# Kernel tuning notes

Hardware: AMD Instinct MI355X
Metric: run time of the kernel (lower is better)

## Reference

```python
import jax, jax.numpy as jnp
import numpy as np

N = 50000
E = 400000
D = 128   # embed_dim == per-head out_channels
H = 2     # graph_heads
NEG_SLOPE = 0.2


def setup_inputs() -> dict:
    key = jax.random.key(0)
    ks = jax.random.split(key, 10)
    s = 1.0 / np.sqrt(D)
    x = jax.random.normal(ks[0], (N, D), dtype=jnp.float32)
    edge_index = jax.random.randint(ks[1], (2, E), 0, N, dtype=jnp.int64)
    # GATv2Conv params: lin_l (source), lin_r (target), attention vector, conv bias
    Wl = jax.random.uniform(ks[2], (H * D, D), jnp.float32, -s, s)
    bl = jax.random.uniform(ks[3], (H * D,), jnp.float32, -s, s)
    Wr = jax.random.uniform(ks[4], (H * D, D), jnp.float32, -s, s)
    br = jax.random.uniform(ks[5], (H * D,), jnp.float32, -s, s)
    att = jax.random.uniform(ks[6], (H, D), jnp.float32, -s, s)
    bias_conv = jnp.zeros((H * D,), jnp.float32)
    # trailing Linear(H*D -> D)
    so = 1.0 / np.sqrt(H * D)
    Wo = jax.random.uniform(ks[7], (D, H * D), jnp.float32, -so, so)
    bo = jax.random.uniform(ks[8], (D,), jnp.float32, -so, so)
    return {"x": x, "edge_index": edge_index, "Wl": Wl, "bl": bl, "Wr": Wr,
            "br": br, "att": att, "bias_conv": bias_conv, "Wo": Wo, "bo": bo}


def reference(x, edge_index, Wl, bl, Wr, br, att, bias_conv, Wo, bo):
    n = x.shape[0]
    # GATv2Conv default add_self_loops=True
    loops = jnp.arange(n, dtype=edge_index.dtype)
    src = jnp.concatenate([edge_index[0], loops])  # x_j (source / message)
    dst = jnp.concatenate([edge_index[1], loops])  # x_i (target / aggregation)

    xl = (x @ Wl.T + bl).reshape(n, H, D)  # source projection
    xr = (x @ Wr.T + br).reshape(n, H, D)  # target projection

    e = xl[src] + xr[dst]                               # [E+N, H, D]
    score = jnp.einsum('ehd,hd->eh', jax.nn.leaky_relu(e, NEG_SLOPE), att)

    # segment softmax over destination neighborhoods
    m = jax.ops.segment_max(score, dst, num_segments=n)  # [N, H]
    a = jnp.exp(score - m[dst])
    denom = jax.ops.segment_sum(a, dst, num_segments=n)
    alpha = a / (denom[dst] + 1e-16)                     # [E+N, H]

    out = jax.ops.segment_sum(xl[src] * alpha[..., None], dst, num_segments=n)
    out = out.reshape(n, H * D) + bias_conv              # concat heads + conv bias
    return out @ Wo.T + bo                               # [N, D]
```

## Files before the change

kernel.cpp:

```cpp
#include <hip/hip_runtime.h>
#include <math.h>

#define DIMV 128
#define HDV  256
#define NEGS 0.2f
#define CAPV 64

typedef __attribute__((ext_vector_type(8))) short short8;
typedef __attribute__((ext_vector_type(8))) unsigned short ushort8v;
typedef __attribute__((ext_vector_type(4))) float f32x4;

__device__ __forceinline__ int edge_at(const int* p, int is64, long long idx) {
    return is64 ? p[2 * idx] : p[(size_t)idx];
}

__device__ __forceinline__ unsigned short f2bf(float f) {
    union { float f; unsigned u; } v; v.f = f;
    unsigned r = (v.u + 0x7FFF + ((v.u >> 16) & 1)) >> 16;
    return (unsigned short)r;
}
__device__ __forceinline__ float bf2f(unsigned short b) {
    union { unsigned u; float f; } v; v.u = ((unsigned)b) << 16;
    return v.f;
}

__global__ __launch_bounds__(256) void build_kernel(
    const int* __restrict__ eidx, int E, int nn,
    int* __restrict__ deg, int* __restrict__ elist)
{
    const int idx = blockIdx.x * 256 + threadIdx.x;
    const int Et = E + nn;
    if (idx >= Et) return;
    const int is64 = ((eidx[1] | eidx[3] | eidx[5] | eidx[7]) == 0) ? 1 : 0;
    int s, d;
    if (idx < E) {
        s = edge_at(eidx, is64, idx);
        d = edge_at(eidx, is64, (long long)E + idx);
    } else {
        s = idx - E; d = s;
    }
    int pos = atomicAdd(deg + d, 1);
    if (pos < CAPV) elist[(size_t)d * CAPV + pos] = s;
}

__global__ __launch_bounds__(256) void prep_kernel(
    const float* __restrict__ Wl, const float* __restrict__ Wr,
    const float* __restrict__ Wo,
    unsigned short* __restrict__ WB, unsigned short* __restrict__ WoB)
{
    const int b = blockIdx.x, t = threadIdx.x;
    if (b < 128) {
        int tid = b * 256 + t;
        int f = tid * 2;
        int e    = f & 7;
        int rowc = (f >> 3) & 127;
        int lg   = (f >> 10) & 3;
        int kk   = (f >> 12) & 3;
        int mh   = f >> 14;
        int mat = mh >> 1, half = mh & 1;
        const float* W = mat ? Wr : Wl;
        float2 v = *(const float2*)(W + (size_t)(half * 128 + rowc) * DIMV + kk * 32 + lg * 8 + e);
        ushort2 o; o.x = f2bf(v.x); o.y = f2bf(v.y);
        *(ushort2*)(WB + f) = o;
    } else {
        int tid = (b - 128) * 256 + t;
        int f = tid * 2;
        int e    = f & 7;
        int rowc = (f >> 3) & 127;
        int lg   = (f >> 10) & 3;
        int kk   = f >> 12;
        float2 v = *(const float2*)(Wo + (size_t)rowc * HDV + kk * 32 + lg * 8 + e);
        ushort2 o; o.x = f2bf(v.x); o.y = f2bf(v.y);
        *(ushort2*)(WoB + f) = o;
    }
}

__global__ __launch_bounds__(512) void proj_mfma_kernel(
    const float* __restrict__ x,
    const unsigned short* __restrict__ WB,
    const float* __restrict__ bl, const float* __restrict__ br,
    unsigned short* __restrict__ xl, unsigned short* __restrict__ xr, int nn)
{
    __shared__ unsigned short xs[64 * 128];
    const int t = threadIdx.x;
    const int m0b = blockIdx.x * 64;
    char* xsb = (char*)xs;

    for (int i = t; i < 64 * 32; i += 512) {
        int rr = i >> 5, q = i & 31;
        float4 v = make_float4(0.f, 0.f, 0.f, 0.f);
        if (m0b + rr < nn) v = ((const float4*)(x + (size_t)(m0b + rr) * DIMV))[q];
        ushort4 bv; bv.x = f2bf(v.x); bv.y = f2bf(v.y); bv.z = f2bf(v.z); bv.w = f2bf(v.w);
        *(ushort4*)(xsb + (((rr * 256) + q * 8) ^ ((rr & 7) << 4))) = bv;
    }
    __syncthreads();

    const int lane = t & 63, w8 = t >> 6;
    const int w = w8 & 3, half = w8 >> 2;
    const int lm = lane & 15, lg = lane >> 4;
    f32x4 acc0[8], acc1[8];
#pragma unroll
    for (int nt = 0; nt < 8; ++nt) {
        acc0[nt] = (f32x4){0.f, 0.f, 0.f, 0.f};
        acc1[nt] = (f32x4){0.f, 0.f, 0.f, 0.f};
    }

    const int arow = w * 16 + lm;
    const int aswz = (arow & 7) << 4;
#pragma unroll
    for (int kk = 0; kk < 4; ++kk) {
        const int koff = kk * 64 + lg * 16;
        short8 afrag = *(const short8*)(xsb + ((arow * 256 + koff) ^ aswz));
        const unsigned short* wb0 = WB + (size_t)(((half * 4 + kk) * 4 + lg) * 128) * 8;
        const unsigned short* wb1 = WB + (size_t)((((2 + half) * 4 + kk) * 4 + lg) * 128) * 8;
#pragma unroll
        for (int nt = 0; nt < 8; ++nt) {
            const int brow = nt * 16 + lm;
            short8 b0 = *(const short8*)(wb0 + brow * 8);
            acc0[nt] = __builtin_amdgcn_mfma_f32_16x16x32_bf16(afrag, b0, acc0[nt], 0, 0, 0);
            short8 b1 = *(const short8*)(wb1 + brow * 8);
            acc1[nt] = __builtin_amdgcn_mfma_f32_16x16x32_bf16(afrag, b1, acc1[nt], 0, 0, 0);
        }
    }

    const int colbase = half * 128;
#pragma unroll
    for (int nt = 0; nt < 8; ++nt) {
        const int c = colbase + nt * 16 + lm;
        const float bv0 = bl[c], bv1 = br[c];
#pragma unroll
        for (int rg = 0; rg < 4; ++rg) {
            const int node = m0b + w * 16 + lg * 4 + rg;
            if (node < nn) {
                xl[(size_t)node * HDV + c] = f2bf(acc0[nt][rg] + bv0);
                xr[(size_t)node * HDV + c] = f2bf(acc1[nt][rg] + bv1);
            }
        }
    }
}

__global__ __launch_bounds__(256) void fused_kernel(
    const unsigned short* __restrict__ xl, const unsigned short* __restrict__ xr,
    const float* __restrict__ att,
    const int* __restrict__ deg, const int* __restrict__ elist,
    const float* __restrict__ bias_conv,
    unsigned short* __restrict__ aggb, int nn)
{
    const int t = threadIdx.x, lane = t & 63, wid = t >> 6;
    const int h = lane & 31, par = lane >> 5;
    const int n0 = blockIdx.x * 16;
    float att8[8], bc8[8];
#pragma unroll
    for (int k = 0; k < 8; ++k) {
        att8[k] = att[h * 8 + k];
        bc8[k]  = bias_conv[h * 8 + k];
    }

    for (int j = 0; j < 4; ++j) {
        const int n = n0 + wid * 4 + j;
        int dg = 0;
        const int* __restrict__ row = elist;
        float xr8[8];
#pragma unroll
        for (int k = 0; k < 8; ++k) xr8[k] = 0.f;
        if (n < nn) {
            dg = min(deg[n], CAPV);
            row = elist + (size_t)n * CAPV;
            ushort8v v = *(const ushort8v*)(xr + (size_t)n * HDV + h * 8);
#pragma unroll
            for (int k = 0; k < 8; ++k) xr8[k] = bf2f(v[k]);
        }
        const int myidx = row[lane];
        const int np = (dg + 1) >> 1, np1 = np - 1, dgm1 = dg - 1;
        float m0 = -1e30f, den = 0.f;
        float a8[8];
#pragma unroll
        for (int k = 0; k < 8; ++k) a8[k] = 0.f;

        if (np > 0) {
            int i0 = __shfl(myidx, min(par, dgm1), 64);
            int i1 = __shfl(myidx, min(2 * min(1, np1) + par, dgm1), 64);
            int i2 = __shfl(myidx, min(2 * min(2, np1) + par, dgm1), 64);
            int i3 = __shfl(myidx, min(2 * min(3, np1) + par, dgm1), 64);
            ushort8v v0 = *(const ushort8v*)(xl + (size_t)i0 * HDV + h * 8);
            ushort8v v1 = *(const ushort8v*)(xl + (size_t)i1 * HDV + h * 8);
            ushort8v v2 = *(const ushort8v*)(xl + (size_t)i2 * HDV + h * 8);
            ushort8v v3 = *(const ushort8v*)(xl + (size_t)i3 * HDV + h * 8);
            for (int ip = 0; ip < np; ++ip) {
                ushort8v cur = v0; v0 = v1; v1 = v2; v2 = v3;
                {
                    int pn = min(2 * min(ip + 4, np1) + par, dgm1);
                    int in_ = __shfl(myidx, pn, 64);
                    v3 = *(const ushort8v*)(xl + (size_t)in_ * HDV + h * 8);
                }
                float xv8[8];
#pragma unroll
                for (int k = 0; k < 8; ++k) xv8[k] = bf2f(cur[k]);
                float p = 0.f;
#pragma unroll
                for (int k = 0; k < 8; ++k) {
                    float e = xv8[k] + xr8[k];
                    e = fmaxf(e, NEGS * e);
                    p = fmaf(e, att8[k], p);
                }
                p += __shfl_xor(p, 1);
                p += __shfl_xor(p, 2);
                p += __shfl_xor(p, 4);
                p += __shfl_xor(p, 8);
                const bool valid = (2 * ip + par) < dg;
                if (!valid) p = -1e30f;
                if (p > m0) {
                    float sc = __expf(m0 - p);
                    den *= sc;
#pragma unroll
                    for (int k = 0; k < 8; ++k) a8[k] *= sc;
                    m0 = p;
                }
                float wgt = valid ? __expf(p - m0) : 0.f;
                den += wgt;
#pragma unroll
                for (int k = 0; k < 8; ++k) a8[k] = fmaf(wgt, xv8[k], a8[k]);
            }
        }
        float m1 = __shfl_xor(m0, 32);
        float d1 = __shfl_xor(den, 32);
        float mm = fmaxf(m0, m1);
        float s0 = __expf(m0 - mm);
        den = den * s0 + d1 * __expf(m1 - mm);
        float rden = 1.f / (den + 1e-16f);
        ushort8v o;
#pragma unroll
        for (int k = 0; k < 8; ++k) {
            float as = a8[k] * s0;
            as += __shfl_xor(as, 32);
            o[k] = f2bf(fmaf(as, rden, bc8[k]));
        }
        if (par == 0 && n < nn)
            *(ushort8v*)(aggb + (size_t)n * HDV + h * 8) = o;
    }
}

__global__ __launch_bounds__(256) void gemm_out_kernel(
    const unsigned short* __restrict__ aggb,
    const unsigned short* __restrict__ WoB,
    const float* __restrict__ bo,
    float* __restrict__ out, int nn)
{
    __shared__ unsigned short xs[64 * 256];
    const int t = threadIdx.x;
    const int m0b = blockIdx.x * 64;
    char* xsb = (char*)xs;

    for (int i = t; i < 64 * 32; i += 256) {
        int rr = i >> 5, q = i & 31;
        ushort8v v = {0, 0, 0, 0, 0, 0, 0, 0};
        if (m0b + rr < nn) v = *(const ushort8v*)(aggb + (size_t)(m0b + rr) * HDV + q * 8);
        *(ushort8v*)(xsb + ((rr * 512 + q * 16) ^ ((rr & 7) << 4))) = v;
    }
    __syncthreads();

    const int lane = t & 63, w = t >> 6;
    const int lm = lane & 15, lg = lane >> 4;
    f32x4 acc[8];
#pragma unroll
    for (int nt = 0; nt < 8; ++nt) acc[nt] = (f32x4){0.f, 0.f, 0.f, 0.f};

    const int arow = w * 16 + lm;
    const int aswz = (arow & 7) << 4;
#pragma unroll
    for (int kk = 0; kk < 8; ++kk) {
        const int koff = kk * 64 + lg * 16;
        short8 afrag = *(const short8*)(xsb + ((arow * 512 + koff) ^ aswz));
        const unsigned short* wb = WoB + (size_t)((kk * 4 + lg) * 128) * 8;
#pragma unroll
        for (int nt = 0; nt < 8; ++nt) {
            const int brow = nt * 16 + lm;
            short8 bfrag = *(const short8*)(wb + brow * 8);
            acc[nt] = __builtin_amdgcn_mfma_f32_16x16x32_bf16(afrag, bfrag, acc[nt], 0, 0, 0);
        }
    }

#pragma unroll
    for (int nt = 0; nt < 8; ++nt) {
        const int c = nt * 16 + lm;
        const float bv = bo[c];
#pragma unroll
        for (int rg = 0; rg < 4; ++rg) {
            const int node = m0b + w * 16 + lg * 4 + rg;
            if (node < nn) out[(size_t)node * DIMV + c] = acc[nt][rg] + bv;
        }
    }
}

extern "C" void kernel_launch(void* const* d_in, const int* in_sizes, int n_in,
                              void* d_out, int out_size, void* d_ws, size_t ws_size,
                              hipStream_t stream) {
    const float* x         = (const float*)d_in[0];
    const int*   eidx      = (const int*)d_in[1];
    const float* Wl        = (const float*)d_in[2];
    const float* bl        = (const float*)d_in[3];
    const float* Wr        = (const float*)d_in[4];
    const float* br        = (const float*)d_in[5];
    const float* att       = (const float*)d_in[6];
    const float* bias_conv = (const float*)d_in[7];
    const float* Wo        = (const float*)d_in[8];
    const float* bo        = (const float*)d_in[9];
    float* out = (float*)d_out;

    const int nn = in_sizes[0] / DIMV;
    const int E  = in_sizes[1] / 2;
    const int Et = E + nn;

    char* ws = (char*)d_ws;
    size_t off = 0;
    auto alloc = [&](size_t bytes) -> void* {
        void* p = ws + off;
        off += (bytes + 255) & ~(size_t)255;
        return p;
    };
    unsigned short* xl   = (unsigned short*)alloc((size_t)nn * HDV * 2);
    unsigned short* xr   = (unsigned short*)alloc((size_t)nn * HDV * 2);
    unsigned short* aggb = (unsigned short*)alloc((size_t)nn * HDV * 2);
    int*   deg   = (int*)alloc((size_t)nn * 4);
    int*   elist = (int*)alloc((size_t)nn * CAPV * 4);
    unsigned short* WB  = (unsigned short*)alloc((size_t)65536 * 2);
    unsigned short* WoB = (unsigned short*)alloc((size_t)32768 * 2);
    (void)ws_size; (void)n_in; (void)out_size;

    hipMemsetAsync(deg, 0, (size_t)nn * 4, stream);

    build_kernel<<<(Et + 255) / 256, 256, 0, stream>>>(eidx, E, nn, deg, elist);

    prep_kernel<<<192, 256, 0, stream>>>(Wl, Wr, Wo, WB, WoB);

    proj_mfma_kernel<<<(nn + 63) / 64, 512, 0, stream>>>(x, WB, bl, br, xl, xr, nn);

    fused_kernel<<<(nn + 15) / 16, 256, 0, stream>>>(xl, xr, att, deg, elist,
                                                     bias_conv, aggb, nn);

    gemm_out_kernel<<<(nn + 63) / 64, 256, 0, stream>>>(aggb, WoB, bo, out, nn);
}
```

Baseline: 141.8 us.

## Merge build and weight-prep kernels; deepen gather prefetch and lazy softmax rescale

Merges the edge-list build and weight bf16 conversion into one launch to save a kernel launch. The aggregation loop now keeps eight neighbour gathers in flight in a rotating register buffer instead of four. It also rescales the online-softmax accumulator only when the new score exceeds the running max by more than 8, which skips rescale work. The bias is now read inside the epilogue rather than held in registers. The larger buffer raises register pressure, and the lazy max lets exponent arguments reach up to e^8, which stays safe in fp32.

```diff
diff --git a/kernel.cpp b/kernel.cpp
--- a/kernel.cpp
+++ b/kernel.cpp
@@ -24,26 +24,9 @@
     return v.f;
 }
 
-__global__ __launch_bounds__(256) void build_kernel(
+__global__ __launch_bounds__(256) void build_prep_kernel(
     const int* __restrict__ eidx, int E, int nn,
-    int* __restrict__ deg, int* __restrict__ elist)
-{
-    const int idx = blockIdx.x * 256 + threadIdx.x;
-    const int Et = E + nn;
-    if (idx >= Et) return;
-    const int is64 = ((eidx[1] | eidx[3] | eidx[5] | eidx[7]) == 0) ? 1 : 0;
-    int s, d;
-    if (idx < E) {
-        s = edge_at(eidx, is64, idx);
-        d = edge_at(eidx, is64, (long long)E + idx);
-    } else {
-        s = idx - E; d = s;
-    }
-    int pos = atomicAdd(deg + d, 1);
-    if (pos < CAPV) elist[(size_t)d * CAPV + pos] = s;
-}
-
-__global__ __launch_bounds__(256) void prep_kernel(
+    int* __restrict__ deg, int* __restrict__ elist,
     const float* __restrict__ Wl, const float* __restrict__ Wr,
     const float* __restrict__ Wo,
     unsigned short* __restrict__ WB, unsigned short* __restrict__ WoB)
@@ -62,7 +45,7 @@
         float2 v = *(const float2*)(W + (size_t)(half * 128 + rowc) * DIMV + kk * 32 + lg * 8 + e);
         ushort2 o; o.x = f2bf(v.x); o.y = f2bf(v.y);
         *(ushort2*)(WB + f) = o;
-    } else {
+    } else if (b < 192) {
         int tid = (b - 128) * 256 + t;
         int f = tid * 2;
         int e    = f & 7;
@@ -72,6 +55,20 @@
         float2 v = *(const float2*)(Wo + (size_t)rowc * HDV + kk * 32 + lg * 8 + e);
         ushort2 o; o.x = f2bf(v.x); o.y = f2bf(v.y);
         *(ushort2*)(WoB + f) = o;
+    } else {
+        const int idx = (b - 192) * 256 + t;
+        const int Et = E + nn;
+        if (idx >= Et) return;
+        const int is64 = ((eidx[1] | eidx[3] | eidx[5] | eidx[7]) == 0) ? 1 : 0;
+        int s, d;
+        if (idx < E) {
+            s = edge_at(eidx, is64, idx);
+            d = edge_at(eidx, is64, (long long)E + idx);
+        } else {
+            s = idx - E; d = s;
+        }
+        int pos = atomicAdd(deg + d, 1);
+        if (pos < CAPV) elist[(size_t)d * CAPV + pos] = s;
     }
 }
 
@@ -149,12 +146,9 @@
     const int t = threadIdx.x, lane = t & 63, wid = t >> 6;
     const int h = lane & 31, par = lane >> 5;
     const int n0 = blockIdx.x * 16;
-    float att8[8], bc8[8];
-#pragma unroll
-    for (int k = 0; k < 8; ++k) {
-        att8[k] = att[h * 8 + k];
-        bc8[k]  = bias_conv[h * 8 + k];
-    }
+    float att8[8];
+#pragma unroll
+    for (int k = 0; k < 8; ++k) att8[k] = att[h * 8 + k];
 
     for (int j = 0; j < 4; ++j) {
         const int n = n0 + wid * 4 + j;
@@ -171,55 +165,60 @@
             for (int k = 0; k < 8; ++k) xr8[k] = bf2f(v[k]);
         }
         const int myidx = row[lane];
-        const int np = (dg + 1) >> 1, np1 = np - 1, dgm1 = dg - 1;
+        const int np = (dg + 1) >> 1, dgm1 = dg - 1;
         float m0 = -1e30f, den = 0.f;
         float a8[8];
 #pragma unroll
         for (int k = 0; k < 8; ++k) a8[k] = 0.f;
 
         if (np > 0) {
-            int i0 = __shfl(myidx, min(par, dgm1), 64);
-            int i1 = __shfl(myidx, min(2 * min(1, np1) + par, dgm1), 64);
-            int i2 = __shfl(myidx, min(2 * min(2, np1) + par, dgm1), 64);
-            int i3 = __shfl(myidx, min(2 * min(3, np1) + par, dgm1), 64);
-            ushort8v v0 = *(const ushort8v*)(xl + (size_t)i0 * HDV + h * 8);
-            ushort8v v1 = *(const ushort8v*)(xl + (size_t)i1 * HDV + h * 8);
-            ushort8v v2 = *(const ushort8v*)(xl + (size_t)i2 * HDV + h * 8);
-            ushort8v v3 = *(const ushort8v*)(xl + (size_t)i3 * HDV + h * 8);
-            for (int ip = 0; ip < np; ++ip) {
-                ushort8v cur = v0; v0 = v1; v1 = v2; v2 = v3;
-                {
-                    int pn = min(2 * min(ip + 4, np1) + par, dgm1);
-                    int in_ = __shfl(myidx, pn, 64);
-                    v3 = *(const ushort8v*)(xl + (size_t)in_ * HDV + h * 8);
+            ushort8v va[8];
+#pragma unroll
+            for (int s = 0; s < 8; ++s) {
+                if (s < np) {
+                    int in_ = __shfl(myidx, min(2 * s + par, dgm1), 64);
+                    va[s] = *(const ushort8v*)(xl + (size_t)in_ * HDV + h * 8);
                 }
-                float xv8[8];
-#pragma unroll
-                for (int k = 0; k < 8; ++k) xv8[k] = bf2f(cur[k]);
-                float p = 0.f;
-#pragma unroll
-                for (int k = 0; k < 8; ++k) {
-                    float e = xv8[k] + xr8[k];
-                    e = fmaxf(e, NEGS * e);
-                    p = fmaf(e, att8[k], p);
+            }
+            for (int base = 0; base < np; base += 8) {
+#pragma unroll
+                for (int s = 0; s < 8; ++s) {
+                    const int ip = base + s;
+                    if (ip < np) {
+                        ushort8v cur = va[s];
+                        if (ip + 8 < np) {
+                            int in_ = __shfl(myidx, min(2 * (ip + 8) + par, dgm1), 64);
+                            va[s] = *(const ushort8v*)(xl + (size_t)in_ * HDV + h * 8);
+                        }
+                        float xv8[8];
+#pragma unroll
+                        for (int k = 0; k < 8; ++k) xv8[k] = bf2f(cur[k]);
+                        float p = 0.f;
+#pragma unroll
+                        for (int k = 0; k < 8; ++k) {
+                            float e = xv8[k] + xr8[k];
+                            e = fmaxf(e, NEGS * e);
+                            p = fmaf(e, att8[k], p);
+                        }
+                        p += __shfl_xor(p, 1);
+                        p += __shfl_xor(p, 2);
+                        p += __shfl_xor(p, 4);
+                        p += __shfl_xor(p, 8);
+                        const bool valid = (2 * ip + par) < dg;
+                        if (!valid) p = -1e30f;
+                        if (p > m0 + 8.f) {
+                            float sc = __expf(m0 - p);
+                            den *= sc;
+#pragma unroll
+                            for (int k = 0; k < 8; ++k) a8[k] *= sc;
+                            m0 = p;
+                        }
+                        float wgt = valid ? __expf(p - m0) : 0.f;
+                        den += wgt;
+#pragma unroll
+                        for (int k = 0; k < 8; ++k) a8[k] = fmaf(wgt, xv8[k], a8[k]);
+                    }
                 }
-                p += __shfl_xor(p, 1);
-                p += __shfl_xor(p, 2);
-                p += __shfl_xor(p, 4);
-                p += __shfl_xor(p, 8);
-                const bool valid = (2 * ip + par) < dg;
-                if (!valid) p = -1e30f;
-                if (p > m0) {
-                    float sc = __expf(m0 - p);
-                    den *= sc;
-#pragma unroll
-                    for (int k = 0; k < 8; ++k) a8[k] *= sc;
-                    m0 = p;
-                }
-                float wgt = valid ? __expf(p - m0) : 0.f;
-                den += wgt;
-#pragma unroll
-                for (int k = 0; k < 8; ++k) a8[k] = fmaf(wgt, xv8[k], a8[k]);
             }
         }
         float m1 = __shfl_xor(m0, 32);
@@ -233,7 +232,7 @@
         for (int k = 0; k < 8; ++k) {
             float as = a8[k] * s0;
             as += __shfl_xor(as, 32);
-            o[k] = f2bf(fmaf(as, rden, bc8[k]));
+            o[k] = f2bf(fmaf(as, rden, bias_conv[h * 8 + k]));
         }
         if (par == 0 && n < nn)
             *(ushort8v*)(aggb + (size_t)n * HDV + h * 8) = o;
@@ -329,9 +328,8 @@
 
     hipMemsetAsync(deg, 0, (size_t)nn * 4, stream);
 
-    build_kernel<<<(Et + 255) / 256, 256, 0, stream>>>(eidx, E, nn, deg, elist);
-
-    prep_kernel<<<192, 256, 0, stream>>>(Wl, Wr, Wo, WB, WoB);
+    build_prep_kernel<<<192 + (Et + 255) / 256, 256, 0, stream>>>(
+        eidx, E, nn, deg, elist, Wl, Wr, Wo, WB, WoB);
 
     proj_mfma_kernel<<<(nn + 63) / 64, 512, 0, stream>>>(x, WB, bl, br, xl, xr, nn);
 
```

Result: slower. 150.5 us (+6.1%).

## Merge build and prep kernels; use 128-row tiles in projection and output GEMMs

Applied to the files above, without the earlier changes.

Folds the edge-list build into the weight-prep kernel so one launch does both. Both MFMA GEMM kernels now process 128 rows per block, and each B fragment loaded from global memory feeds two row groups, halving weight-fragment traffic per row. The projection kernel also handles the two weight matrices one after another instead of together. The cost is fewer blocks (about 391), double the LDS per block (32 or 64 KB), and a higher accumulator register count in gemm_out, which can reduce occupancy.

```diff
diff --git a/kernel.cpp b/kernel.cpp
--- a/kernel.cpp
+++ b/kernel.cpp
@@ -24,26 +24,9 @@
     return v.f;
 }
 
-__global__ __launch_bounds__(256) void build_kernel(
+__global__ __launch_bounds__(256) void build_prep_kernel(
     const int* __restrict__ eidx, int E, int nn,
-    int* __restrict__ deg, int* __restrict__ elist)
-{
-    const int idx = blockIdx.x * 256 + threadIdx.x;
-    const int Et = E + nn;
-    if (idx >= Et) return;
-    const int is64 = ((eidx[1] | eidx[3] | eidx[5] | eidx[7]) == 0) ? 1 : 0;
-    int s, d;
-    if (idx < E) {
-        s = edge_at(eidx, is64, idx);
-        d = edge_at(eidx, is64, (long long)E + idx);
-    } else {
-        s = idx - E; d = s;
-    }
-    int pos = atomicAdd(deg + d, 1);
-    if (pos < CAPV) elist[(size_t)d * CAPV + pos] = s;
-}
-
-__global__ __launch_bounds__(256) void prep_kernel(
+    int* __restrict__ deg, int* __restrict__ elist,
     const float* __restrict__ Wl, const float* __restrict__ Wr,
     const float* __restrict__ Wo,
     unsigned short* __restrict__ WB, unsigned short* __restrict__ WoB)
@@ -62,7 +45,7 @@
         float2 v = *(const float2*)(W + (size_t)(half * 128 + rowc) * DIMV + kk * 32 + lg * 8 + e);
         ushort2 o; o.x = f2bf(v.x); o.y = f2bf(v.y);
         *(ushort2*)(WB + f) = o;
-    } else {
+    } else if (b < 192) {
         int tid = (b - 128) * 256 + t;
         int f = tid * 2;
         int e    = f & 7;
@@ -72,6 +55,20 @@
         float2 v = *(const float2*)(Wo + (size_t)rowc * HDV + kk * 32 + lg * 8 + e);
         ushort2 o; o.x = f2bf(v.x); o.y = f2bf(v.y);
         *(ushort2*)(WoB + f) = o;
+    } else {
+        const int idx = (b - 192) * 256 + t;
+        const int Et = E + nn;
+        if (idx >= Et) return;
+        const int is64 = ((eidx[1] | eidx[3] | eidx[5] | eidx[7]) == 0) ? 1 : 0;
+        int s, d;
+        if (idx < E) {
+            s = edge_at(eidx, is64, idx);
+            d = edge_at(eidx, is64, (long long)E + idx);
+        } else {
+            s = idx - E; d = s;
+        }
+        int pos = atomicAdd(deg + d, 1);
+        if (pos < CAPV) elist[(size_t)d * CAPV + pos] = s;
     }
 }
 
@@ -81,12 +78,12 @@
     const float* __restrict__ bl, const float* __restrict__ br,
     unsigned short* __restrict__ xl, unsigned short* __restrict__ xr, int nn)
 {
-    __shared__ unsigned short xs[64 * 128];
+    __shared__ unsigned short xs[128 * 128];
     const int t = threadIdx.x;
-    const int m0b = blockIdx.x * 64;
+    const int m0b = blockIdx.x * 128;
     char* xsb = (char*)xs;
 
-    for (int i = t; i < 64 * 32; i += 512) {
+    for (int i = t; i < 128 * 32; i += 512) {
         int rr = i >> 5, q = i & 31;
         float4 v = make_float4(0.f, 0.f, 0.f, 0.f);
         if (m0b + rr < nn) v = ((const float4*)(x + (size_t)(m0b + rr) * DIMV))[q];
@@ -96,44 +93,49 @@
     __syncthreads();
 
     const int lane = t & 63, w8 = t >> 6;
-    const int w = w8 & 3, half = w8 >> 2;
+    const int wsub = w8 & 3, half = w8 >> 2;
     const int lm = lane & 15, lg = lane >> 4;
-    f32x4 acc0[8], acc1[8];
-#pragma unroll
-    for (int nt = 0; nt < 8; ++nt) {
-        acc0[nt] = (f32x4){0.f, 0.f, 0.f, 0.f};
-        acc1[nt] = (f32x4){0.f, 0.f, 0.f, 0.f};
-    }
-
-    const int arow = w * 16 + lm;
-    const int aswz = (arow & 7) << 4;
-#pragma unroll
-    for (int kk = 0; kk < 4; ++kk) {
-        const int koff = kk * 64 + lg * 16;
-        short8 afrag = *(const short8*)(xsb + ((arow * 256 + koff) ^ aswz));
-        const unsigned short* wb0 = WB + (size_t)(((half * 4 + kk) * 4 + lg) * 128) * 8;
-        const unsigned short* wb1 = WB + (size_t)((((2 + half) * 4 + kk) * 4 + lg) * 128) * 8;
+    const int arowA = wsub * 16 + lm;
+    const int arowB = 64 + wsub * 16 + lm;
+    const int swzA = (arowA & 7) << 4;
+    const int swzB = (arowB & 7) << 4;
+    const int colbase = half * 128;
+
+    for (int mat = 0; mat < 2; ++mat) {
+        f32x4 acc[2][8];
+#pragma unroll
+        for (int g = 0; g < 2; ++g)
+#pragma unroll
+            for (int nt = 0; nt < 8; ++nt) acc[g][nt] = (f32x4){0.f, 0.f, 0.f, 0.f};
+
+#pragma unroll
+        for (int kk = 0; kk < 4; ++kk) {
+            const int koff = kk * 64 + lg * 16;
+            short8 afA = *(const short8*)(xsb + ((arowA * 256 + koff) ^ swzA));
+            short8 afB = *(const short8*)(xsb + ((arowB * 256 + koff) ^ swzB));
+            const unsigned short* wb =
+                WB + (size_t)((((mat * 2 + half) * 4 + kk) * 4 + lg) * 128) * 8;
+#pragma unroll
+            for (int nt = 0; nt < 8; ++nt) {
+                short8 bfrag = *(const short8*)(wb + (nt * 16 + lm) * 8);
+                acc[0][nt] = __builtin_amdgcn_mfma_f32_16x16x32_bf16(afA, bfrag, acc[0][nt], 0, 0, 0);
+                acc[1][nt] = __builtin_amdgcn_mfma_f32_16x16x32_bf16(afB, bfrag, acc[1][nt], 0, 0, 0);
+            }
+        }
+
+        const float* __restrict__ bias = mat ? br : bl;
+        unsigned short* __restrict__ o = mat ? xr : xl;
 #pragma unroll
         for (int nt = 0; nt < 8; ++nt) {
-            const int brow = nt * 16 + lm;
-            short8 b0 = *(const short8*)(wb0 + brow * 8);
-            acc0[nt] = __builtin_amdgcn_mfma_f32_16x16x32_bf16(afrag, b0, acc0[nt], 0, 0, 0);
-            short8 b1 = *(const short8*)(wb1 + brow * 8);
-            acc1[nt] = __builtin_amdgcn_mfma_f32_16x16x32_bf16(afrag, b1, acc1[nt], 0, 0, 0);
-        }
-    }
-
-    const int colbase = half * 128;
-#pragma unroll
-    for (int nt = 0; nt < 8; ++nt) {
-        const int c = colbase + nt * 16 + lm;
-        const float bv0 = bl[c], bv1 = br[c];
-#pragma unroll
-        for (int rg = 0; rg < 4; ++rg) {
-            const int node = m0b + w * 16 + lg * 4 + rg;
-            if (node < nn) {
-                xl[(size_t)node * HDV + c] = f2bf(acc0[nt][rg] + bv0);
-                xr[(size_t)node * HDV + c] = f2bf(acc1[nt][rg] + bv1);
+            const int c = colbase + nt * 16 + lm;
+            const float bv = bias[c];
+#pragma unroll
+            for (int g = 0; g < 2; ++g) {
+#pragma unroll
+                for (int rg = 0; rg < 4; ++rg) {
+                    const int node = m0b + g * 64 + wsub * 16 + lg * 4 + rg;
+                    if (node < nn) o[(size_t)node * HDV + c] = f2bf(acc[g][nt][rg] + bv);
+                }
             }
         }
     }
@@ -246,12 +248,12 @@
     const float* __restrict__ bo,
     float* __restrict__ out, int nn)
 {
-    __shared__ unsigned short xs[64 * 256];
+    __shared__ unsigned short xs[128 * 256];
     const int t = threadIdx.x;
-    const int m0b = blockIdx.x * 64;
+    const int m0b = blockIdx.x * 128;
     char* xsb = (char*)xs;
 
-    for (int i = t; i < 64 * 32; i += 256) {
+    for (int i = t; i < 128 * 32; i += 256) {
         int rr = i >> 5, q = i & 31;
         ushort8v v = {0, 0, 0, 0, 0, 0, 0, 0};
         if (m0b + rr < nn) v = *(const ushort8v*)(aggb + (size_t)(m0b + rr) * HDV + q * 8);
@@ -261,22 +263,27 @@
 
     const int lane = t & 63, w = t >> 6;
     const int lm = lane & 15, lg = lane >> 4;
-    f32x4 acc[8];
-#pragma unroll
-    for (int nt = 0; nt < 8; ++nt) acc[nt] = (f32x4){0.f, 0.f, 0.f, 0.f};
-
-    const int arow = w * 16 + lm;
-    const int aswz = (arow & 7) << 4;
+    const int arowA = w * 16 + lm;
+    const int arowB = 64 + w * 16 + lm;
+    const int swzA = (arowA & 7) << 4;
+    const int swzB = (arowB & 7) << 4;
+    f32x4 acc[2][8];
+#pragma unroll
+    for (int g = 0; g < 2; ++g)
+#pragma unroll
+        for (int nt = 0; nt < 8; ++nt) acc[g][nt] = (f32x4){0.f, 0.f, 0.f, 0.f};
+
 #pragma unroll
     for (int kk = 0; kk < 8; ++kk) {
         const int koff = kk * 64 + lg * 16;
-        short8 afrag = *(const short8*)(xsb + ((arow * 512 + koff) ^ aswz));
+        short8 afA = *(const short8*)(xsb + ((arowA * 512 + koff) ^ swzA));
+        short8 afB = *(const short8*)(xsb + ((arowB * 512 + koff) ^ swzB));
         const unsigned short* wb = WoB + (size_t)((kk * 4 + lg) * 128) * 8;
 #pragma unroll
         for (int nt = 0; nt < 8; ++nt) {
-            const int brow = nt * 16 + lm;
-            short8 bfrag = *(const short8*)(wb + brow * 8);
-            acc[nt] = __builtin_amdgcn_mfma_f32_16x16x32_bf16(afrag, bfrag, acc[nt], 0, 0, 0);
+            short8 bfrag = *(const short8*)(wb + (nt * 16 + lm) * 8);
+            acc[0][nt] = __builtin_amdgcn_mfma_f32_16x16x32_bf16(afA, bfrag, acc[0][nt], 0, 0, 0);
+            acc[1][nt] = __builtin_amdgcn_mfma_f32_16x16x32_bf16(afB, bfrag, acc[1][nt], 0, 0, 0);
         }
     }
 
@@ -285,9 +292,12 @@
         const int c = nt * 16 + lm;
         const float bv = bo[c];
 #pragma unroll
-        for (int rg = 0; rg < 4; ++rg) {
-            const int node = m0b + w * 16 + lg * 4 + rg;
-            if (node < nn) out[(size_t)node * DIMV + c] = acc[nt][rg] + bv;
+        for (int g = 0; g < 2; ++g) {
+#pragma unroll
+            for (int rg = 0; rg < 4; ++rg) {
+                const int node = m0b + g * 64 + w * 16 + lg * 4 + rg;
+                if (node < nn) out[(size_t)node * DIMV + c] = acc[g][nt][rg] + bv;
+            }
         }
     }
 }
@@ -329,14 +339,13 @@
 
     hipMemsetAsync(deg, 0, (size_t)nn * 4, stream);
 
-    build_kernel<<<(Et + 255) / 256, 256, 0, stream>>>(eidx, E, nn, deg, elist);
-
-    prep_kernel<<<192, 256, 0, stream>>>(Wl, Wr, Wo, WB, WoB);
-
-    proj_mfma_kernel<<<(nn + 63) / 64, 512, 0, stream>>>(x, WB, bl, br, xl, xr, nn);
+    build_prep_kernel<<<192 + (Et + 255) / 256, 256, 0, stream>>>(
+        eidx, E, nn, deg, elist, Wl, Wr, Wo, WB, WoB);
+
+    proj_mfma_kernel<<<(nn + 127) / 128, 512, 0, stream>>>(x, WB, bl, br, xl, xr, nn);
 
     fused_kernel<<<(nn + 15) / 16, 256, 0, stream>>>(xl, xr, att, deg, elist,
                                                      bias_conv, aggb, nn);
 
-    gemm_out_kernel<<<(nn + 63) / 64, 256, 0, stream>>>(aggb, WoB, bo, out, nn);
-}
+    gemm_out_kernel<<<(nn + 127) / 128, 256, 0, stream>>>(aggb, WoB, bo, out, nn);
+}
```

Result: slower. 162.5 us (+14.6%).

## Merge edge build with weight prep, stage projection stores via LDS, widen fused blocks

Applied to the files above, without the earlier changes.

Folds the edge-list build and the weight bf16 conversion into a single launch, which removes one kernel launch. The projection epilogue now writes bf16 results into a shared-memory tile and then stores them as coalesced 16-byte row vectors, replacing scattered 2-byte stores. This costs an extra 32KB of LDS per block, which may lower occupancy. The aggregation kernel now uses 512-thread blocks covering 32 nodes each.

```diff
diff --git a/kernel.cpp b/kernel.cpp
--- a/kernel.cpp
+++ b/kernel.cpp
@@ -24,26 +24,9 @@
     return v.f;
 }
 
-__global__ __launch_bounds__(256) void build_kernel(
+__global__ __launch_bounds__(256) void build_prep_kernel(
     const int* __restrict__ eidx, int E, int nn,
-    int* __restrict__ deg, int* __restrict__ elist)
-{
-    const int idx = blockIdx.x * 256 + threadIdx.x;
-    const int Et = E + nn;
-    if (idx >= Et) return;
-    const int is64 = ((eidx[1] | eidx[3] | eidx[5] | eidx[7]) == 0) ? 1 : 0;
-    int s, d;
-    if (idx < E) {
-        s = edge_at(eidx, is64, idx);
-        d = edge_at(eidx, is64, (long long)E + idx);
-    } else {
-        s = idx - E; d = s;
-    }
-    int pos = atomicAdd(deg + d, 1);
-    if (pos < CAPV) elist[(size_t)d * CAPV + pos] = s;
-}
-
-__global__ __launch_bounds__(256) void prep_kernel(
+    int* __restrict__ deg, int* __restrict__ elist,
     const float* __restrict__ Wl, const float* __restrict__ Wr,
     const float* __restrict__ Wo,
     unsigned short* __restrict__ WB, unsigned short* __restrict__ WoB)
@@ -62,7 +45,7 @@
         float2 v = *(const float2*)(W + (size_t)(half * 128 + rowc) * DIMV + kk * 32 + lg * 8 + e);
         ushort2 o; o.x = f2bf(v.x); o.y = f2bf(v.y);
         *(ushort2*)(WB + f) = o;
-    } else {
+    } else if (b < 192) {
         int tid = (b - 128) * 256 + t;
         int f = tid * 2;
         int e    = f & 7;
@@ -72,6 +55,20 @@
         float2 v = *(const float2*)(Wo + (size_t)rowc * HDV + kk * 32 + lg * 8 + e);
         ushort2 o; o.x = f2bf(v.x); o.y = f2bf(v.y);
         *(ushort2*)(WoB + f) = o;
+    } else {
+        const int idx = (b - 192) * 256 + t;
+        const int Et = E + nn;
+        if (idx >= Et) return;
+        const int is64 = ((eidx[1] | eidx[3] | eidx[5] | eidx[7]) == 0) ? 1 : 0;
+        int s, d;
+        if (idx < E) {
+            s = edge_at(eidx, is64, idx);
+            d = edge_at(eidx, is64, (long long)E + idx);
+        } else {
+            s = idx - E; d = s;
+        }
+        int pos = atomicAdd(deg + d, 1);
+        if (pos < CAPV) elist[(size_t)d * CAPV + pos] = s;
     }
 }
 
@@ -81,7 +78,8 @@
     const float* __restrict__ bl, const float* __restrict__ br,
     unsigned short* __restrict__ xl, unsigned short* __restrict__ xr, int nn)
 {
-    __shared__ unsigned short xs[64 * 128];
+    __shared__ __align__(16) unsigned short xs[64 * 128];
+    __shared__ __align__(16) unsigned short os[64 * 256];
     const int t = threadIdx.x;
     const int m0b = blockIdx.x * 64;
     char* xsb = (char*)xs;
@@ -127,19 +125,37 @@
 #pragma unroll
     for (int nt = 0; nt < 8; ++nt) {
         const int c = colbase + nt * 16 + lm;
-        const float bv0 = bl[c], bv1 = br[c];
-#pragma unroll
-        for (int rg = 0; rg < 4; ++rg) {
-            const int node = m0b + w * 16 + lg * 4 + rg;
-            if (node < nn) {
-                xl[(size_t)node * HDV + c] = f2bf(acc0[nt][rg] + bv0);
-                xr[(size_t)node * HDV + c] = f2bf(acc1[nt][rg] + bv1);
-            }
-        }
-    }
-}
-
-__global__ __launch_bounds__(256) void fused_kernel(
+        const float bv = bl[c];
+#pragma unroll
+        for (int rg = 0; rg < 4; ++rg)
+            os[(w * 16 + lg * 4 + rg) * 256 + c] = f2bf(acc0[nt][rg] + bv);
+    }
+    __syncthreads();
+    for (int i = t; i < 64 * 32; i += 512) {
+        int rr = i >> 5, q = i & 31;
+        if (m0b + rr < nn)
+            *(ushort8v*)(xl + (size_t)(m0b + rr) * HDV + q * 8) =
+                *(const ushort8v*)(os + rr * 256 + q * 8);
+    }
+    __syncthreads();
+#pragma unroll
+    for (int nt = 0; nt < 8; ++nt) {
+        const int c = colbase + nt * 16 + lm;
+        const float bv = br[c];
+#pragma unroll
+        for (int rg = 0; rg < 4; ++rg)
+            os[(w * 16 + lg * 4 + rg) * 256 + c] = f2bf(acc1[nt][rg] + bv);
+    }
+    __syncthreads();
+    for (int i = t; i < 64 * 32; i += 512) {
+        int rr = i >> 5, q = i & 31;
+        if (m0b + rr < nn)
+            *(ushort8v*)(xr + (size_t)(m0b + rr) * HDV + q * 8) =
+                *(const ushort8v*)(os + rr * 256 + q * 8);
+    }
+}
+
+__global__ __launch_bounds__(512) void fused_kernel(
     const unsigned short* __restrict__ xl, const unsigned short* __restrict__ xr,
     const float* __restrict__ att,
     const int* __restrict__ deg, const int* __restrict__ elist,
@@ -148,7 +164,7 @@
 {
     const int t = threadIdx.x, lane = t & 63, wid = t >> 6;
     const int h = lane & 31, par = lane >> 5;
-    const int n0 = blockIdx.x * 16;
+    const int n0 = blockIdx.x * 32;
     float att8[8], bc8[8];
 #pragma unroll
     for (int k = 0; k < 8; ++k) {
@@ -246,7 +262,7 @@
     const float* __restrict__ bo,
     float* __restrict__ out, int nn)
 {
-    __shared__ unsigned short xs[64 * 256];
+    __shared__ __align__(16) unsigned short xs[64 * 256];
     const int t = threadIdx.x;
     const int m0b = blockIdx.x * 64;
     char* xsb = (char*)xs;
@@ -329,13 +345,12 @@
 
     hipMemsetAsync(deg, 0, (size_t)nn * 4, stream);
 
-    build_kernel<<<(Et + 255) / 256, 256, 0, stream>>>(eidx, E, nn, deg, elist);
-
-    prep_kernel<<<192, 256, 0, stream>>>(Wl, Wr, Wo, WB, WoB);
+    build_prep_kernel<<<192 + (Et + 255) / 256, 256, 0, stream>>>(
+        eidx, E, nn, deg, elist, Wl, Wr, Wo, WB, WoB);
 
     proj_mfma_kernel<<<(nn + 63) / 64, 512, 0, stream>>>(x, WB, bl, br, xl, xr, nn);
 
-    fused_kernel<<<(nn + 15) / 16, 256, 0, stream>>>(xl, xr, att, deg, elist,
+    fused_kernel<<<(nn + 31) / 32, 512, 0, stream>>>(xl, xr, att, deg, elist,
                                                      bias_conv, aggb, nn);
 
     gemm_out_kernel<<<(nn + 63) / 64, 256, 0, stream>>>(aggb, WoB, bo, out, nn);
```

Result: slower. 147.2 us (+3.8%).
